# Performance work log

Measured on AMD Instinct MI355X. Metric: run time of the kernel, lower is better.

Reference implementation:

```python
import jax, jax.numpy as jnp
import numpy as np

PLP_ORDER = 16
N_CHANNEL = 40
FFT_LENGTH = 512
SAMPLE_RATE = 16000
LIFTER = 22
COMP_FACTOR = 0.33
FLOOR = 1e-5
F_MIN = 0.0
F_MAX = SAMPLE_RATE / 2


def _hz_to_mel(hz):
    return 1127.0 * np.log1p(np.asarray(hz, dtype=np.float64) / 700.0)


def _mel_to_hz(mel):
    return 700.0 * np.expm1(np.asarray(mel, dtype=np.float64) / 1127.0)


def _build_constants():
    # SPTK-style mel filter bank (triangular in mel domain).
    mel_min = _hz_to_mel(F_MIN)
    mel_max = _hz_to_mel(F_MAX)
    lower_bin = max(1, int(F_MIN / SAMPLE_RATE * FFT_LENGTH + 1.5))
    upper_bin = min(FFT_LENGTH // 2, int(F_MAX / SAMPLE_RATE * FFT_LENGTH + 0.5))
    seed = np.arange(1, N_CHANNEL + 2)
    cf_mel = (mel_max - mel_min) / (N_CHANNEL + 1) * seed + mel_min  # (C+1,)
    bins = np.arange(lower_bin, upper_bin)
    mel = _hz_to_mel(SAMPLE_RATE * bins / FFT_LENGTH)
    ch = np.searchsorted(cf_mel, mel, side='left')  # first center freq >= mel
    diff = cf_mel - np.concatenate([[mel_min], cf_mel[:-1]])
    w = (cf_mel[ch] - mel) / diff[ch]
    H = np.zeros((len(bins), N_CHANNEL))
    rows = np.arange(len(bins))
    low = ch - 1
    m_lo = low >= 0
    H[rows[m_lo], low[m_lo]] += w[m_lo]
    m_hi = ch <= N_CHANNEL - 1
    H[rows[m_hi], ch[m_hi]] += 1.0 - w[m_hi]
    # Equal-loudness curve over the first C center frequencies (in Hz).
    cf_hz = _mel_to_hz(cf_mel)
    f2 = cf_hz[:N_CHANNEL] ** 2
    eql = (f2 / (f2 + 160000.0)) ** 2 * (f2 + 1440000.0) / (f2 + 9610000.0)
    # Liftering vector, v[0] = 2.
    m = np.arange(PLP_ORDER + 1)
    lift = 1.0 + LIFTER / 2.0 * np.sin(np.pi / LIFTER * m)
    lift[0] = 2.0
    return lower_bin, upper_bin, H.astype(np.float32), eql.astype(np.float32), lift.astype(np.float32)


LOWER_BIN, UPPER_BIN, H_NP, EQL_NP, LIFT_NP = _build_constants()


def _levinson_durbin(r):
    # r: (..., M+1) autocorrelation -> (gain K, LPC coefficients a_1..a_M)
    M = PLP_ORDER
    E = r[..., 0]
    a = jnp.zeros(r.shape[:-1] + (M,), r.dtype)
    for i in range(1, M + 1):
        acc = r[..., i]
        if i > 1:
            acc = acc + jnp.einsum('...j,...j->...', a[..., : i - 1], r[..., 1:i][..., ::-1])
        k = -acc / E
        if i > 1:
            a = a.at[..., : i - 1].set(a[..., : i - 1] + k[..., None] * a[..., : i - 1][..., ::-1])
        a = a.at[..., i - 1].set(k)
        E = E * (1.0 - k * k)
    return jnp.sqrt(E), a


def _lpc_to_cepstrum(K, a):
    # c0 = log K; c_m = -a_m - sum_{k=1}^{m-1} (k/m) c_k a_{m-k}
    M = PLP_ORDER
    c = [jnp.log(K)]
    for m in range(1, M + 1):
        acc = a[..., m - 1]
        for k in range(1, m):
            acc = acc + (k / m) * c[k] * a[..., m - k - 1]
        c.append(-acc)
    return jnp.stack(c, axis=-1)  # (..., M+1)


def _plp(x):
    H = jnp.asarray(H_NP)
    eql = jnp.asarray(EQL_NP)
    lift = jnp.asarray(LIFT_NP)
    # Mel filter bank on power spectrum (use_power=True)
    fb = jnp.matmul(x[..., LOWER_BIN:UPPER_BIN], H)          # (..., C)
    logfb = jnp.log(jnp.maximum(fb, FLOOR))
    # Equal-loudness scaling + cubic-root amplitude compression
    y = (jnp.exp(logfb) * eql) ** COMP_FACTOR                # (..., C)
    # replicate1: duplicate first and last channels
    y = jnp.concatenate([y[..., :1], y, y[..., -1:]], axis=-1)  # (..., C+2)
    n = y.shape[-1]
    # hfft with norm='forward' -> inverse-FFT-like autocorrelation
    r = jnp.fft.hfft(y) / (2 * (n - 1))
    r = r[..., : PLP_ORDER + 1]
    K, a = _levinson_durbin(r)
    c = _lpc_to_cepstrum(K, a)
    c = c * lift
    return c[..., 1:]  # out_format 'y': PLP without C0, (..., M)


def setup_inputs() -> dict:
    key = jax.random.key(0)
    x = jax.random.uniform(key, (32, 4096, FFT_LENGTH // 2 + 1), dtype=jnp.float32)
    return {"x": x}


def reference(x):
    return _plp(x)
```

## Files before the change

### kernel.cpp

```cpp
#include <hip/hip_runtime.h>
#include <hip/hip_fp16.h>

#define NCH    40
#define MORD   16
#define NR     17
#define NBINS  257
#define FPB    128

namespace cfg {

constexpr double PI  = 3.14159265358979323846264338327950288;
constexpr double LN2 = 0.693147180559945309417232121458176568;

constexpr double cexp(double x) {
    double t = 1.0, s = 1.0;
    for (int i = 1; i < 40; ++i) { t *= x / i; s += t; }
    return s;
}

constexpr double clog(double z) {
    double lg = 0.0;
    while (z > 1.4142135623730951) { z *= 0.5; lg += LN2; }
    while (z < 0.7071067811865476) { z *= 2.0; lg -= LN2; }
    double u = (z - 1.0) / (z + 1.0), u2 = u * u, t = u, s = u;
    for (int k = 1; k < 24; ++k) { t *= u2; s += t / (2.0 * k + 1.0); }
    return lg + 2.0 * s;
}

constexpr double ccos(double x) {
    double tp = 2.0 * PI;
    double q = x / tp;
    long long k = (long long)(q + (q >= 0.0 ? 0.5 : -0.5));
    double r = x - (double)k * tp;
    double r2 = r * r, t = 1.0, s = 1.0;
    for (int i = 1; i < 20; ++i) { t *= -r2 / ((2.0 * i - 1.0) * (2.0 * i)); s += t; }
    return s;
}

constexpr double csin(double x) { return ccos(x - PI / 2.0); }

struct Tab {
    int   start[43];
    int   chan[257];
    float w[257];
    float eql[NCH];
    float lift[NR];
    float ctf[NR][21];
    constexpr Tab() : start(), chan(), w(), eql(), lift(), ctf() {
        const double lmax  = clog(87.0 / 7.0);
        const double U1127 = lmax / 41.0;
        for (int c = 0; c <= 41; ++c) {
            double thr = 22.4 * (cexp((double)c * U1127) - 1.0);
            int s = (int)thr + 1;
            if (s < 1) s = 1;
            if (s > 256) s = 256;
            start[c] = s;
        }
        start[42] = start[41];
        for (int c = 0; c <= 40; ++c) {
            for (int b = start[c]; b < start[c + 1]; ++b) {
                double mel = 1127.0 * clog(1.0 + (double)b * 31.25 / 700.0);
                double t   = mel / (1127.0 * U1127);
                w[b] = (float)(t - (double)c);
                chan[b] = c;
            }
        }
        for (int c = 0; c < NCH; ++c) {
            double cf = 700.0 * (cexp((double)(c + 1) * U1127) - 1.0);
            double f2 = cf * cf;
            double e  = f2 / (f2 + 160000.0);
            e = e * e * (f2 + 1440000.0) / (f2 + 9610000.0);
            eql[c] = (float)e;
        }
        for (int m = 0; m < NR; ++m)
            lift[m] = (float)(1.0 + 11.0 * csin(PI * (double)m / 22.0));
        lift[0] = 2.0f;
        for (int l = 0; l < NR; ++l)
            for (int j = 0; j <= 20; ++j) {
                double s = (j == 0) ? 1.0 : 2.0;
                ctf[l][j] = (float)(s * ccos(PI * (double)(j * l) / 41.0) / 82.0);
            }
    }
};

constexpr Tab T{};

}

template<int PAR>
__device__ __forceinline__ void fbank_pairs(const __half2* __restrict__ fr2, float fb[NCH])
{
    using cfg::T;
    #pragma unroll
    for (int p = 0; p < 128; ++p) {
        const float2 xp = __half22float2(fr2[p]);
        {
            const int   bb = 2 * p + PAR;
            const int   ch = T.chan[bb];
            const float wa = T.w[bb];
            if (wa != 0.f || ch != 0) {
                if (ch < NCH) fb[ch]     = fmaf(wa, xp.x, fb[ch]);
                if (ch >= 1)  fb[ch - 1] = fmaf(1.0f - wa, xp.x, fb[ch - 1]);
            }
        }
        {
            const int   bb = 2 * p + 1 + PAR;
            const int   ch = T.chan[bb];
            const float wa = T.w[bb];
            if (wa != 0.f || ch != 0) {
                if (ch < NCH) fb[ch]     = fmaf(wa, xp.y, fb[ch]);
                if (ch >= 1)  fb[ch - 1] = fmaf(1.0f - wa, xp.y, fb[ch - 1]);
            }
        }
    }
}

__global__ __launch_bounds__(FPB) void plp_kernel(const float* __restrict__ x,
                                                  float* __restrict__ out,
                                                  int nframes)
{
    using cfg::T;
    __shared__ __half slabH[FPB * NBINS];

    const int tid = threadIdx.x;
    const long long F0 = (long long)blockIdx.x * FPB;

    {
        const float4* src = reinterpret_cast<const float4*>(x + F0 * NBINS);
        #pragma unroll 8
        for (int r = 0; r < 64; ++r) {
            const int i = (r << 7) + tid;
            const float4 v = src[i];
            union { __half2 h[2]; uint2 u; } cv;
            cv.h[0] = __float22half2_rn(make_float2(v.x, v.y));
            cv.h[1] = __float22half2_rn(make_float2(v.z, v.w));
            *reinterpret_cast<uint2*>(&slabH[(size_t)4 * i]) = cv.u;
        }
        if (tid < 32) {
            const int i = 8192 + tid;
            const float4 v = src[i];
            union { __half2 h[2]; uint2 u; } cv;
            cv.h[0] = __float22half2_rn(make_float2(v.x, v.y));
            cv.h[1] = __float22half2_rn(make_float2(v.z, v.w));
            *reinterpret_cast<uint2*>(&slabH[(size_t)4 * i]) = cv.u;
        }
    }
    __syncthreads();

    const int w  = tid >> 6;
    const int l  = tid & 63;
    const int fl = 2 * l + w;
    const long long frame = F0 + fl;

    const __half2* fr2 = reinterpret_cast<const __half2*>(&slabH[fl * NBINS + w]);

    float fb[NCH];
    #pragma unroll
    for (int c = 0; c < NCH; ++c) fb[c] = 0.f;

    if (w == 0) fbank_pairs<0>(fr2, fb);
    else        fbank_pairs<1>(fr2, fb);

    float yv[NCH];
    #pragma unroll
    for (int c = 0; c < NCH; ++c) {
        float v = fmaxf(fb[c], 1e-5f) * T.eql[c];
        yv[c] = __expf(0.33f * __logf(v));
    }

    float ye[21], yo[21];
    ye[0] = yv[0] + yv[39];  yo[0] = yv[0] - yv[39];
    #pragma unroll
    for (int jj = 1; jj <= 20; ++jj) {
        float aa = yv[jj - 1], bb = yv[40 - jj];
        ye[jj] = aa + bb;  yo[jj] = aa - bb;
    }

    float rr[NR];
    #pragma unroll
    for (int lg = 0; lg < NR; ++lg) {
        const float* yy = (lg & 1) ? yo : ye;
        float acc = 0.f;
        #pragma unroll
        for (int jj = 0; jj <= 20; ++jj) acc = fmaf(T.ctf[lg][jj], yy[jj], acc);
        rr[lg] = acc;
    }

    float a[MORD];
    #pragma unroll
    for (int i = 0; i < MORD; ++i) a[i] = 0.f;
    float E = rr[0];
    #pragma unroll
    for (int i = 1; i <= MORD; ++i) {
        float acc = rr[i];
        #pragma unroll
        for (int jj = 0; jj < i - 1; ++jj) acc = fmaf(a[jj], rr[i - 1 - jj], acc);
        float k = -acc * __builtin_amdgcn_rcpf(E);
        const int half = (i - 1) / 2;
        #pragma unroll
        for (int jj = 0; jj < half; ++jj) {
            float t1 = a[jj], t2 = a[i - 2 - jj];
            a[jj]         = fmaf(k, t2, t1);
            a[i - 2 - jj] = fmaf(k, t1, t2);
        }
        if ((i - 1) & 1) a[half] = fmaf(k, a[half], a[half]);
        a[i - 1] = k;
        E = E * (1.f - k * k);
    }

    float cc[NR], ccs[NR];
    #pragma unroll
    for (int m = 1; m <= MORD; ++m) {
        float acc = 0.f;
        #pragma unroll
        for (int k2 = 1; k2 < m; ++k2)
            acc = fmaf(ccs[k2], a[m - k2 - 1], acc);
        float cm = -(a[m - 1] + acc * (1.0f / (float)m));
        cc[m]  = cm;
        ccs[m] = (float)m * cm;
    }

    if (frame < (long long)nframes) {
        float o[16];
        #pragma unroll
        for (int m = 1; m <= MORD; ++m) o[m - 1] = cc[m] * T.lift[m];

        float4* op = reinterpret_cast<float4*>(out + (size_t)frame * 16);
        op[0] = make_float4(o[0],  o[1],  o[2],  o[3]);
        op[1] = make_float4(o[4],  o[5],  o[6],  o[7]);
        op[2] = make_float4(o[8],  o[9],  o[10], o[11]);
        op[3] = make_float4(o[12], o[13], o[14], o[15]);
    }
}

extern "C" void kernel_launch(void* const* d_in, const int* in_sizes, int n_in,
                              void* d_out, int out_size, void* d_ws, size_t ws_size,
                              hipStream_t stream) {
    const float* x   = (const float*)d_in[0];
    float*      outp = (float*)d_out;
    int nframes = in_sizes[0] / NBINS;
    int nblocks = (nframes + FPB - 1) / FPB;
    plp_kernel<<<nblocks, FPB, 0, stream>>>(x, outp, nframes);
}
```

Baseline: 196.3 us.

## Warp-specialize loader and compute waves with double-buffered LDS across frame chunks

The block grows to 256 threads and four waves are specialized. Two waves stream the next 128-frame chunk from global memory into one half of a double-buffered half-precision LDS slab, using register prefetch. The other two waves compute PLP on the previous chunk from the other half. Each block now handles four chunks, so loads overlap compute. In exchange LDS use doubles to about 131 KB per block, which lowers occupancy, and half the waves sit idle in each phase.

```diff
diff --git a/kernel.cpp b/kernel.cpp
--- a/kernel.cpp
+++ b/kernel.cpp
@@ -5,7 +5,9 @@
 #define MORD   16
 #define NR     17
 #define NBINS  257
-#define FPB    128
+#define TPB    256
+#define CFRM   128
+#define GENS   4
 
 namespace cfg {
 
@@ -115,121 +117,155 @@
     }
 }
 
-__global__ __launch_bounds__(FPB) void plp_kernel(const float* __restrict__ x,
+__global__ __launch_bounds__(TPB) void plp_kernel(const float* __restrict__ x,
                                                   float* __restrict__ out,
                                                   int nframes)
 {
     using cfg::T;
-    __shared__ __half slabH[FPB * NBINS];
+    __shared__ __half slabH[2][CFRM * NBINS];
 
     const int tid = threadIdx.x;
-    const long long F0 = (long long)blockIdx.x * FPB;
-
-    {
-        const float4* src = reinterpret_cast<const float4*>(x + F0 * NBINS);
-        #pragma unroll 8
-        for (int r = 0; r < 64; ++r) {
-            const int i = (r << 7) + tid;
-            const float4 v = src[i];
-            union { __half2 h[2]; uint2 u; } cv;
-            cv.h[0] = __float22half2_rn(make_float2(v.x, v.y));
-            cv.h[1] = __float22half2_rn(make_float2(v.z, v.w));
-            *reinterpret_cast<uint2*>(&slabH[(size_t)4 * i]) = cv.u;
-        }
-        if (tid < 32) {
-            const int i = 8192 + tid;
-            const float4 v = src[i];
-            union { __half2 h[2]; uint2 u; } cv;
-            cv.h[0] = __float22half2_rn(make_float2(v.x, v.y));
-            cv.h[1] = __float22half2_rn(make_float2(v.z, v.w));
-            *reinterpret_cast<uint2*>(&slabH[(size_t)4 * i]) = cv.u;
-        }
-    }
-    __syncthreads();
-
-    const int w  = tid >> 6;
-    const int l  = tid & 63;
-    const int fl = 2 * l + w;
-    const long long frame = F0 + fl;
-
-    const __half2* fr2 = reinterpret_cast<const __half2*>(&slabH[fl * NBINS + w]);
-
-    float fb[NCH];
-    #pragma unroll
-    for (int c = 0; c < NCH; ++c) fb[c] = 0.f;
-
-    if (w == 0) fbank_pairs<0>(fr2, fb);
-    else        fbank_pairs<1>(fr2, fb);
-
-    float yv[NCH];
-    #pragma unroll
-    for (int c = 0; c < NCH; ++c) {
-        float v = fmaxf(fb[c], 1e-5f) * T.eql[c];
-        yv[c] = __expf(0.33f * __logf(v));
-    }
-
-    float ye[21], yo[21];
-    ye[0] = yv[0] + yv[39];  yo[0] = yv[0] - yv[39];
-    #pragma unroll
-    for (int jj = 1; jj <= 20; ++jj) {
-        float aa = yv[jj - 1], bb = yv[40 - jj];
-        ye[jj] = aa + bb;  yo[jj] = aa - bb;
-    }
-
-    float rr[NR];
-    #pragma unroll
-    for (int lg = 0; lg < NR; ++lg) {
-        const float* yy = (lg & 1) ? yo : ye;
-        float acc = 0.f;
-        #pragma unroll
-        for (int jj = 0; jj <= 20; ++jj) acc = fmaf(T.ctf[lg][jj], yy[jj], acc);
-        rr[lg] = acc;
-    }
-
-    float a[MORD];
-    #pragma unroll
-    for (int i = 0; i < MORD; ++i) a[i] = 0.f;
-    float E = rr[0];
-    #pragma unroll
-    for (int i = 1; i <= MORD; ++i) {
-        float acc = rr[i];
-        #pragma unroll
-        for (int jj = 0; jj < i - 1; ++jj) acc = fmaf(a[jj], rr[i - 1 - jj], acc);
-        float k = -acc * __builtin_amdgcn_rcpf(E);
-        const int half = (i - 1) / 2;
-        #pragma unroll
-        for (int jj = 0; jj < half; ++jj) {
-            float t1 = a[jj], t2 = a[i - 2 - jj];
-            a[jj]         = fmaf(k, t2, t1);
-            a[i - 2 - jj] = fmaf(k, t1, t2);
-        }
-        if ((i - 1) & 1) a[half] = fmaf(k, a[half], a[half]);
-        a[i - 1] = k;
-        E = E * (1.f - k * k);
-    }
-
-    float cc[NR], ccs[NR];
-    #pragma unroll
-    for (int m = 1; m <= MORD; ++m) {
-        float acc = 0.f;
-        #pragma unroll
-        for (int k2 = 1; k2 < m; ++k2)
-            acc = fmaf(ccs[k2], a[m - k2 - 1], acc);
-        float cm = -(a[m - 1] + acc * (1.0f / (float)m));
-        cc[m]  = cm;
-        ccs[m] = (float)m * cm;
-    }
-
-    if (frame < (long long)nframes) {
-        float o[16];
-        #pragma unroll
-        for (int m = 1; m <= MORD; ++m) o[m - 1] = cc[m] * T.lift[m];
-
-        float4* op = reinterpret_cast<float4*>(out + (size_t)frame * 16);
-        op[0] = make_float4(o[0],  o[1],  o[2],  o[3]);
-        op[1] = make_float4(o[4],  o[5],  o[6],  o[7]);
-        op[2] = make_float4(o[8],  o[9],  o[10], o[11]);
-        op[3] = make_float4(o[12], o[13], o[14], o[15]);
+    const int w   = tid >> 6;
+    const long long B0    = (long long)blockIdx.x * (CFRM * GENS);
+    const long long i4max = ((long long)nframes * NBINS) >> 2;
+
+    #pragma unroll 1
+    for (int ph = 0; ph <= GENS; ++ph) {
+        if (ph < GENS && w < 2) {
+            const int st = tid;
+            const long long Fg    = B0 + (long long)ph * CFRM;
+            const long long base4 = (Fg * NBINS) >> 2;
+            const float4* src4 = reinterpret_cast<const float4*>(x);
+            uint2* dst = reinterpret_cast<uint2*>(&slabH[ph & 1][0]);
+
+            float4 cur[8];
+            #pragma unroll
+            for (int k = 0; k < 8; ++k) {
+                long long gi = base4 + k * 128 + st;
+                cur[k] = src4[gi < i4max ? gi : (i4max - 1)];
+            }
+            #pragma unroll
+            for (int grp = 0; grp < 8; ++grp) {
+                float4 nxt[8];
+                if (grp < 7) {
+                    #pragma unroll
+                    for (int k = 0; k < 8; ++k) {
+                        long long gi = base4 + (grp + 1) * 1024 + k * 128 + st;
+                        nxt[k] = src4[gi < i4max ? gi : (i4max - 1)];
+                    }
+                }
+                #pragma unroll
+                for (int k = 0; k < 8; ++k) {
+                    const int i = grp * 1024 + k * 128 + st;
+                    union { __half2 h[2]; uint2 u; } cv;
+                    cv.h[0] = __float22half2_rn(make_float2(cur[k].x, cur[k].y));
+                    cv.h[1] = __float22half2_rn(make_float2(cur[k].z, cur[k].w));
+                    dst[i] = cv.u;
+                }
+                if (grp < 7) {
+                    #pragma unroll
+                    for (int k = 0; k < 8; ++k) cur[k] = nxt[k];
+                }
+            }
+            if (st < 32) {
+                long long gi = base4 + 8192 + st;
+                const float4 v = src4[gi < i4max ? gi : (i4max - 1)];
+                union { __half2 h[2]; uint2 u; } cv;
+                cv.h[0] = __float22half2_rn(make_float2(v.x, v.y));
+                cv.h[1] = __float22half2_rn(make_float2(v.z, v.w));
+                dst[8192 + st] = cv.u;
+            }
+        }
+
+        if (ph > 0 && w >= 2) {
+            const int g   = ph - 1;
+            const int par = w - 2;
+            const int l   = tid & 63;
+            const int fl  = 2 * l + par;
+            const long long frame = B0 + (long long)g * CFRM + fl;
+            const __half2* fr2 = reinterpret_cast<const __half2*>(
+                &slabH[g & 1][fl * NBINS + par]);
+
+            float fb[NCH];
+            #pragma unroll
+            for (int c = 0; c < NCH; ++c) fb[c] = 0.f;
+
+            if (par == 0) fbank_pairs<0>(fr2, fb);
+            else          fbank_pairs<1>(fr2, fb);
+
+            float yv[NCH];
+            #pragma unroll
+            for (int c = 0; c < NCH; ++c) {
+                float v = fmaxf(fb[c], 1e-5f) * T.eql[c];
+                yv[c] = __expf(0.33f * __logf(v));
+            }
+
+            float ye[21], yo[21];
+            ye[0] = yv[0] + yv[39];  yo[0] = yv[0] - yv[39];
+            #pragma unroll
+            for (int jj = 1; jj <= 20; ++jj) {
+                float aa = yv[jj - 1], bb = yv[40 - jj];
+                ye[jj] = aa + bb;  yo[jj] = aa - bb;
+            }
+
+            float rr[NR];
+            #pragma unroll
+            for (int lg = 0; lg < NR; ++lg) {
+                const float* yy = (lg & 1) ? yo : ye;
+                float acc = 0.f;
+                #pragma unroll
+                for (int jj = 0; jj <= 20; ++jj) acc = fmaf(T.ctf[lg][jj], yy[jj], acc);
+                rr[lg] = acc;
+            }
+
+            float a[MORD];
+            #pragma unroll
+            for (int i = 0; i < MORD; ++i) a[i] = 0.f;
+            float E = rr[0];
+            #pragma unroll
+            for (int i = 1; i <= MORD; ++i) {
+                float acc = rr[i];
+                #pragma unroll
+                for (int jj = 0; jj < i - 1; ++jj) acc = fmaf(a[jj], rr[i - 1 - jj], acc);
+                float k = -acc * __builtin_amdgcn_rcpf(E);
+                const int half = (i - 1) / 2;
+                #pragma unroll
+                for (int jj = 0; jj < half; ++jj) {
+                    float t1 = a[jj], t2 = a[i - 2 - jj];
+                    a[jj]         = fmaf(k, t2, t1);
+                    a[i - 2 - jj] = fmaf(k, t1, t2);
+                }
+                if ((i - 1) & 1) a[half] = fmaf(k, a[half], a[half]);
+                a[i - 1] = k;
+                E = E * (1.f - k * k);
+            }
+
+            float cc[NR], ccs[NR];
+            #pragma unroll
+            for (int m = 1; m <= MORD; ++m) {
+                float acc = 0.f;
+                #pragma unroll
+                for (int k2 = 1; k2 < m; ++k2)
+                    acc = fmaf(ccs[k2], a[m - k2 - 1], acc);
+                float cm = -(a[m - 1] + acc * (1.0f / (float)m));
+                cc[m]  = cm;
+                ccs[m] = (float)m * cm;
+            }
+
+            if (frame < (long long)nframes) {
+                float o[16];
+                #pragma unroll
+                for (int m = 1; m <= MORD; ++m) o[m - 1] = cc[m] * T.lift[m];
+
+                float4* op = reinterpret_cast<float4*>(out + (size_t)frame * 16);
+                op[0] = make_float4(o[0],  o[1],  o[2],  o[3]);
+                op[1] = make_float4(o[4],  o[5],  o[6],  o[7]);
+                op[2] = make_float4(o[8],  o[9],  o[10], o[11]);
+                op[3] = make_float4(o[12], o[13], o[14], o[15]);
+            }
+        }
+
+        __syncthreads();
     }
 }
 
@@ -239,6 +275,6 @@
     const float* x   = (const float*)d_in[0];
     float*      outp = (float*)d_out;
     int nframes = in_sizes[0] / NBINS;
-    int nblocks = (nframes + FPB - 1) / FPB;
-    plp_kernel<<<nblocks, FPB, 0, stream>>>(x, outp, nframes);
-}
+    int nblocks = (nframes + CFRM * GENS - 1) / (CFRM * GENS);
+    plp_kernel<<<nblocks, TPB, 0, stream>>>(x, outp, nframes);
+}
```

Result: slower. 200.6 us (+2.2%).
